# Performance work log

Measured on AMD Instinct MI355X. Metric: run time of the kernel, lower is better.

## Reference

```python
import jax, jax.numpy as jnp
import numpy as np
import math

B, S, H, NH = 2, 2048, 1024, 16
DH = H // NH  # 64
REL_VOCAB = 4096  # 2 * (max_position_embeddings // 4)


def setup_inputs() -> dict:
    key = jax.random.key(0)
    ks = jax.random.split(key, 9)
    s = 0.02
    return {
        "hidden_states": jax.random.normal(ks[0], (B, S, H), jnp.float32),
        "attention_mask": jnp.zeros((B, 1, 1, S), jnp.float32),
        "distance_idx": jax.random.randint(ks[1], (S, S), 0, REL_VOCAB),
        "Wq": jax.random.normal(ks[2], (H, H), jnp.float32) * s,
        "bq": jnp.zeros((H,), jnp.float32),
        "Wk": jax.random.normal(ks[3], (H, H), jnp.float32) * s,
        "bk": jnp.zeros((H,), jnp.float32),
        "Wv": jax.random.normal(ks[4], (H, H), jnp.float32) * s,
        "bv": jnp.zeros((H,), jnp.float32),
        "dist_emb": jax.random.normal(ks[5], (REL_VOCAB, NH), jnp.float32) * s,
    }


def _heads(x):
    # [B,S,H] -> [B,NH,S,DH]
    return x.reshape(B, S, NH, DH).transpose(0, 2, 1, 3)


def reference(hidden_states, attention_mask, distance_idx, Wq, bq, Wk, bk, Wv, bv, dist_emb):
    q = _heads(hidden_states @ Wq.T + bq)
    k = _heads(hidden_states @ Wk.T + bk)
    v = _heads(hidden_states @ Wv.T + bv)
    # scores: [B,NH,S,S]
    scores = jnp.einsum("bhqd,bhkd->bhqk", q, k) / math.sqrt(DH)
    # relative_scalar_bias: embed(distance_idx) [S,S,NH] -> [1,NH,S,S]
    bias = dist_emb[distance_idx].transpose(2, 0, 1)[None]
    scores = scores + bias  # attention_scores_terms == 1 -> /sqrt(1)
    scores = scores + attention_mask
    probs = jax.nn.softmax(scores, axis=-1)
    ctx = jnp.einsum("bhqk,bhkd->bhqd", probs, v)
    return ctx.transpose(0, 2, 1, 3).reshape(B, S, H)
```

## Files before the change

### kernel.cpp

```cpp
#include <hip/hip_runtime.h>
#include <hip/hip_bf16.h>

#define B_   2
#define S_   2048
#define H_   1024
#define NH_  16
#define DH_  64

typedef __attribute__((ext_vector_type(8))) __bf16 bf16x8;
typedef __attribute__((ext_vector_type(8))) unsigned short u16x8;
typedef __attribute__((ext_vector_type(4))) float f32x4;

typedef const __attribute__((address_space(1))) unsigned int gu32_t;
typedef __attribute__((address_space(3))) unsigned int su32_t;

static __device__ inline unsigned short f2bf(float x) {
    union { float f; unsigned u; } v; v.f = x;
    unsigned r = v.u + 0x7fffu + ((v.u >> 16) & 1u);
    return (unsigned short)(r >> 16);
}

static __device__ inline unsigned short f2bf_r(float x) {
    union { float f; unsigned u; } v; v.f = x;
    return (unsigned short)((v.u + 0x8000u) >> 16);
}

static __device__ inline float bf2f(unsigned short u) {
    union { unsigned u; float f; } v; v.u = ((unsigned)u) << 16;
    return v.f;
}

static __device__ inline bf16x8 ldfrag(const unsigned short* p) {
    return __builtin_bit_cast(bf16x8, *(const u16x8*)p);
}

__global__ void conv_all(const float* __restrict__ x,
                         const float* __restrict__ Wq, const float* __restrict__ Wk,
                         const float* __restrict__ Wv, const float* __restrict__ demb,
                         unsigned short* __restrict__ xb, unsigned short* __restrict__ wall,
                         unsigned short* __restrict__ dembT) {
    int bid = blockIdx.x, tid = threadIdx.x;
    if (bid < 4096) {
        int i = bid * 256 + tid;
        float4 v = ((const float4*)x)[i];
        ushort4 o;
        o.x = f2bf(v.x); o.y = f2bf(v.y); o.z = f2bf(v.z); o.w = f2bf(v.w);
        ((ushort4*)xb)[i] = o;
    } else if (bid < 7168) {
        int i = (bid - 4096) * 256 + tid;
        int e = i * 4;
        int which = e >> 20;
        int r4 = (e & ((1 << 20) - 1)) >> 2;
        const float* src = which == 0 ? Wq : which == 1 ? Wk : Wv;
        float4 v = ((const float4*)src)[r4];
        ushort4 o;
        o.x = f2bf(v.x); o.y = f2bf(v.y); o.z = f2bf(v.z); o.w = f2bf(v.w);
        ((ushort4*)wall)[i] = o;
    } else {
        int t = (bid - 7168) * 256 + tid;
        int h = t >> 12, e = t & 4095;
        dembT[t] = f2bf(demb[e * 16 + h]);
    }
}

__global__ __launch_bounds__(256) void gemm_qkv(
    const unsigned short* __restrict__ Xb, const unsigned short* __restrict__ Wall,
    const float* __restrict__ bq, const float* __restrict__ bk, const float* __restrict__ bv,
    unsigned short* __restrict__ Q, unsigned short* __restrict__ K, unsigned short* __restrict__ V)
{
    __shared__ unsigned short As[128 * 32];
    __shared__ unsigned short Bs[128 * 32];
    const int tid = threadIdx.x, lane = tid & 63, wv = tid >> 6;
    const int g = lane >> 4, l16 = lane & 15;
    const int wm = wv >> 1, wn = wv & 1;
    const int bm = blockIdx.y, bn = blockIdx.x;

    const int lrow = lane >> 2, lcol = (lane & 3) * 8;

    f32x4 acc[4][4];
    #pragma unroll
    for (int i = 0; i < 4; ++i)
        #pragma unroll
        for (int j = 0; j < 4; ++j) acc[i][j] = (f32x4){0.f, 0.f, 0.f, 0.f};

    for (int kt = 0; kt < 32; ++kt) {
        #pragma unroll
        for (int i = 0; i < 2; ++i) {
            int chunk = wv * 2 + i;
            int row = chunk * 16 + lrow;
            const unsigned short* ga = &Xb[(size_t)(bm * 128 + row) * 1024 + kt * 32 + lcol];
            const unsigned short* gb = &Wall[(size_t)(bn * 128 + row) * 1024 + kt * 32 + lcol];
            __builtin_amdgcn_global_load_lds((gu32_t*)(const void*)ga, (su32_t*)(void*)&As[chunk * 512], 16, 0, 0);
            __builtin_amdgcn_global_load_lds((gu32_t*)(const void*)gb, (su32_t*)(void*)&Bs[chunk * 512], 16, 0, 0);
        }
        __syncthreads();
        bf16x8 a[4], b[4];
        #pragma unroll
        for (int mi = 0; mi < 4; ++mi) a[mi] = ldfrag(&As[(wm * 64 + mi * 16 + l16) * 32 + g * 8]);
        #pragma unroll
        for (int ni = 0; ni < 4; ++ni) b[ni] = ldfrag(&Bs[(wn * 64 + ni * 16 + l16) * 32 + g * 8]);
        #pragma unroll
        for (int mi = 0; mi < 4; ++mi)
            #pragma unroll
            for (int ni = 0; ni < 4; ++ni)
                acc[mi][ni] = __builtin_amdgcn_mfma_f32_16x16x32_bf16(a[mi], b[ni], acc[mi][ni], 0, 0, 0);
        __syncthreads();
    }

    #pragma unroll
    for (int mi = 0; mi < 4; ++mi) {
        #pragma unroll
        for (int ni = 0; ni < 4; ++ni) {
            int gn = bn * 128 + wn * 64 + ni * 16 + l16;
            int which = gn >> 10, nn = gn & 1023;
            int h = nn >> 6, d = nn & 63;
            float bias = which == 0 ? bq[nn] : which == 1 ? bk[nn] : bv[nn];
            unsigned short* dst = which == 0 ? Q : which == 1 ? K : V;
            #pragma unroll
            for (int r = 0; r < 4; ++r) {
                int gm = bm * 128 + wm * 64 + mi * 16 + g * 4 + r;
                int bb = gm >> 11, s = gm & 2047;
                dst[((size_t)(bb * 16 + h) * 2048 + s) * 64 + d] = f2bf(acc[mi][ni][r] + bias);
            }
        }
    }
}

__global__ void transpose_v(const unsigned short* __restrict__ V, unsigned short* __restrict__ VT) {
    __shared__ unsigned short t[64][65];
    int bh = blockIdx.y, st = blockIdx.x, tid = threadIdx.x;
    size_t ib = (size_t)bh * S_ * DH_ + (size_t)st * 64 * 64;
    #pragma unroll
    for (int rep = 0; rep < 16; ++rep) {
        int e = rep * 256 + tid;
        t[e >> 6][e & 63] = V[ib + e];
    }
    __syncthreads();
    size_t ob = (size_t)bh * DH_ * S_ + st * 64;
    #pragma unroll
    for (int rep = 0; rep < 16; ++rep) {
        int e = rep * 256 + tid;
        int d = e >> 6, sl = e & 63;
        VT[ob + (size_t)d * S_ + sl] = t[sl][d];
    }
}

__global__ __launch_bounds__(256, 4) void attn(
    const unsigned short* __restrict__ Q, const unsigned short* __restrict__ K,
    const unsigned short* __restrict__ VT, const int* __restrict__ didx,
    const unsigned short* __restrict__ dembT, const float* __restrict__ mask,
    float* __restrict__ out)
{
    __shared__ unsigned short demb_h[4096];
    __shared__ unsigned short Ks[64 * 64];
    __shared__ unsigned short Vs[64 * 64];
    __shared__ unsigned short Ps[4][16 * 64];
    const int tid = threadIdx.x, lane = tid & 63, w = tid >> 6;
    const int g = lane >> 4, l16 = lane & 15;
    const int h = blockIdx.x, qt = blockIdx.y, b = blockIdx.z;
    const int bh = b * NH_ + h;
    const int qr = qt * 64 + w * 16;

    #pragma unroll
    for (int j = 0; j < 2; ++j) {
        int i = j * 256 + tid;
        *(uint4*)&demb_h[i * 8] = *(const uint4*)&dembT[h * 4096 + i * 8];
    }

    bf16x8 qf[2];
    {
        size_t qbase = ((size_t)bh * S_ + qr + l16) * DH_;
        qf[0] = ldfrag(&Q[qbase + g * 8]);
        qf[1] = ldfrag(&Q[qbase + 32 + g * 8]);
    }

    f32x4 oa[4];
    float lsum[4];
    #pragma unroll
    for (int i = 0; i < 4; ++i) {
        oa[i] = (f32x4){0.f, 0.f, 0.f, 0.f};
        lsum[i] = 0.f;
    }

    const size_t kbase = (size_t)bh * S_ * DH_;
    const size_t vbase = (size_t)bh * DH_ * S_;

    __syncthreads();

    for (int kt = 0; kt < 32; ++kt) {
        #pragma unroll
        for (int j = 0; j < 2; ++j) {
            int e = j * 2048 + tid * 8;
            int r = e >> 6, c = e & 63;
            int sidx = r * 64 + ((((c >> 3) ^ (r & 7))) << 3);
            *(uint4*)&Ks[sidx] = *(const uint4*)&K[kbase + (size_t)kt * 64 * 64 + e];
            *(uint4*)&Vs[sidx] = *(const uint4*)&VT[vbase + (size_t)r * S_ + kt * 64 + c];
        }

        int ei[4][4];
        float mk[4];
        #pragma unroll
        for (int kj = 0; kj < 4; ++kj) {
            int kg = kt * 64 + kj * 16 + l16;
            mk[kj] = mask[b * S_ + kg];
            #pragma unroll
            for (int r = 0; r < 4; ++r) {
                int qg = qr + g * 4 + r;
                ei[kj][r] = didx[qg * S_ + kg];
            }
        }

        __syncthreads();

        f32x4 sc[4];
        #pragma unroll
        for (int kj = 0; kj < 4; ++kj) {
            int row = kj * 16 + l16, m = row & 7;
            bf16x8 kf0 = ldfrag(&Ks[row * 64 + ((g ^ m) << 3)]);
            bf16x8 kf1 = ldfrag(&Ks[row * 64 + (((g + 4) ^ m) << 3)]);
            f32x4 z = (f32x4){0.f, 0.f, 0.f, 0.f};
            z = __builtin_amdgcn_mfma_f32_16x16x32_bf16(qf[0], kf0, z, 0, 0, 0);
            z = __builtin_amdgcn_mfma_f32_16x16x32_bf16(qf[1], kf1, z, 0, 0, 0);
            sc[kj] = z;
        }

        #pragma unroll
        for (int kj = 0; kj < 4; ++kj) {
            #pragma unroll
            for (int r = 0; r < 4; ++r) {
                float bm = bf2f(demb_h[ei[kj][r]]) + mk[kj];
                float p = __expf(fmaf(sc[kj][r], 0.125f, bm));
                lsum[r] += p;
                int row = g * 4 + r;
                int idx = row * 64 + ((((kj * 2 + (l16 >> 3)) ^ (row & 7))) << 3) + (l16 & 7);
                Ps[w][idx] = f2bf_r(p);
            }
        }

        int pm = l16 & 7;
        bf16x8 pf0 = ldfrag(&Ps[w][l16 * 64 + ((g ^ pm) << 3)]);
        bf16x8 pf1 = ldfrag(&Ps[w][l16 * 64 + (((g + 4) ^ pm) << 3)]);
        #pragma unroll
        for (int dt = 0; dt < 4; ++dt) {
            int row = dt * 16 + l16, m = row & 7;
            bf16x8 vf0 = ldfrag(&Vs[row * 64 + ((g ^ m) << 3)]);
            bf16x8 vf1 = ldfrag(&Vs[row * 64 + (((g + 4) ^ m) << 3)]);
            oa[dt] = __builtin_amdgcn_mfma_f32_16x16x32_bf16(pf0, vf0, oa[dt], 0, 0, 0);
            oa[dt] = __builtin_amdgcn_mfma_f32_16x16x32_bf16(pf1, vf1, oa[dt], 0, 0, 0);
        }
        __syncthreads();
    }

    float linv[4];
    #pragma unroll
    for (int r = 0; r < 4; ++r) {
        float s = lsum[r];
        s += __shfl_xor(s, 1);
        s += __shfl_xor(s, 2);
        s += __shfl_xor(s, 4);
        s += __shfl_xor(s, 8);
        linv[r] = __builtin_amdgcn_rcpf(s);
    }

    #pragma unroll
    for (int dt = 0; dt < 4; ++dt) {
        #pragma unroll
        for (int r = 0; r < 4; ++r) {
            int s = qr + g * 4 + r;
            int d = dt * 16 + l16;
            out[((size_t)b * S_ + s) * H_ + h * DH_ + d] = oa[dt][r] * linv[r];
        }
    }
}

extern "C" void kernel_launch(void* const* d_in, const int* in_sizes, int n_in,
                              void* d_out, int out_size, void* d_ws, size_t ws_size,
                              hipStream_t stream) {
    const float* hidden = (const float*)d_in[0];
    const float* mask   = (const float*)d_in[1];
    const int*   didx   = (const int*)d_in[2];
    const float* Wq     = (const float*)d_in[3];
    const float* bq     = (const float*)d_in[4];
    const float* Wk     = (const float*)d_in[5];
    const float* bk     = (const float*)d_in[6];
    const float* Wv     = (const float*)d_in[7];
    const float* bv     = (const float*)d_in[8];
    const float* demb   = (const float*)d_in[9];
    float* out = (float*)d_out;

    unsigned short* ws = (unsigned short*)d_ws;
    unsigned short* Xb   = ws;
    unsigned short* Wall = Xb + 4096 * 1024;
    unsigned short* Qb   = Wall + 3072 * 1024;
    unsigned short* Kb   = Qb + 4194304;
    unsigned short* Vb   = Kb + 4194304;
    unsigned short* VTb  = Vb + 4194304;
    unsigned short* DembT = VTb + 4194304;

    conv_all<<<7424, 256, 0, stream>>>(hidden, Wq, Wk, Wv, demb, Xb, Wall, DembT);
    gemm_qkv<<<dim3(24, 32), 256, 0, stream>>>(Xb, Wall, bq, bk, bv, Qb, Kb, Vb);
    transpose_v<<<dim3(32, 32), 256, 0, stream>>>(Vb, VTb);
    attn<<<dim3(16, 32, 2), 256, 0, stream>>>(Qb, Kb, VTb, didx, DembT, mask, out);
}
```

Baseline: 221.4 us.

## Register-prefetch next K/V tile and bias indices; raise wave priority around MFMAs

```diff
diff --git a/kernel.cpp b/kernel.cpp
--- a/kernel.cpp
+++ b/kernel.cpp
@@ -185,6 +185,32 @@
     const size_t kbase = (size_t)bh * S_ * DH_;
     const size_t vbase = (size_t)bh * DH_ * S_;
 
+    uint4 kreg[2], vreg[2];
+    int   ei[4][4];
+    float mk[4];
+
+    auto load_kv = [&](int kt) {
+        #pragma unroll
+        for (int j = 0; j < 2; ++j) {
+            int e = j * 2048 + tid * 8;
+            int r = e >> 6, c = e & 63;
+            kreg[j] = *(const uint4*)&K[kbase + (size_t)kt * 64 * 64 + e];
+            vreg[j] = *(const uint4*)&VT[vbase + (size_t)r * S_ + kt * 64 + c];
+        }
+    };
+
+    load_kv(0);
+    #pragma unroll
+    for (int kj = 0; kj < 4; ++kj) {
+        int kg = kj * 16 + l16;
+        mk[kj] = mask[b * S_ + kg];
+        #pragma unroll
+        for (int r = 0; r < 4; ++r) {
+            int qg = qr + g * 4 + r;
+            ei[kj][r] = didx[qg * S_ + kg];
+        }
+    }
+
     __syncthreads();
 
     for (int kt = 0; kt < 32; ++kt) {
@@ -193,26 +219,35 @@
             int e = j * 2048 + tid * 8;
             int r = e >> 6, c = e & 63;
             int sidx = r * 64 + ((((c >> 3) ^ (r & 7))) << 3);
-            *(uint4*)&Ks[sidx] = *(const uint4*)&K[kbase + (size_t)kt * 64 * 64 + e];
-            *(uint4*)&Vs[sidx] = *(const uint4*)&VT[vbase + (size_t)r * S_ + kt * 64 + c];
-        }
-
-        int ei[4][4];
-        float mk[4];
+            *(uint4*)&Ks[sidx] = kreg[j];
+            *(uint4*)&Vs[sidx] = vreg[j];
+        }
+        __syncthreads();
+
+        const int ktn = (kt + 1) & 31;
+        load_kv(ktn);
+        int ein[4][4];
+        float mkn[4];
         #pragma unroll
         for (int kj = 0; kj < 4; ++kj) {
-            int kg = kt * 64 + kj * 16 + l16;
-            mk[kj] = mask[b * S_ + kg];
+            int kg = ktn * 64 + kj * 16 + l16;
+            mkn[kj] = mask[b * S_ + kg];
             #pragma unroll
             for (int r = 0; r < 4; ++r) {
                 int qg = qr + g * 4 + r;
-                ei[kj][r] = didx[qg * S_ + kg];
+                ein[kj][r] = didx[qg * S_ + kg];
             }
         }
 
-        __syncthreads();
+        float bm[4][4];
+        #pragma unroll
+        for (int kj = 0; kj < 4; ++kj)
+            #pragma unroll
+            for (int r = 0; r < 4; ++r)
+                bm[kj][r] = bf2f(demb_h[ei[kj][r]]) + mk[kj];
 
         f32x4 sc[4];
+        __builtin_amdgcn_s_setprio(1);
         #pragma unroll
         for (int kj = 0; kj < 4; ++kj) {
             int row = kj * 16 + l16, m = row & 7;
@@ -223,13 +258,13 @@
             z = __builtin_amdgcn_mfma_f32_16x16x32_bf16(qf[1], kf1, z, 0, 0, 0);
             sc[kj] = z;
         }
+        __builtin_amdgcn_s_setprio(0);
 
         #pragma unroll
         for (int kj = 0; kj < 4; ++kj) {
             #pragma unroll
             for (int r = 0; r < 4; ++r) {
-                float bm = bf2f(demb_h[ei[kj][r]]) + mk[kj];
-                float p = __expf(fmaf(sc[kj][r], 0.125f, bm));
+                float p = __expf(fmaf(sc[kj][r], 0.125f, bm[kj][r]));
                 lsum[r] += p;
                 int row = g * 4 + r;
                 int idx = row * 64 + ((((kj * 2 + (l16 >> 3)) ^ (row & 7))) << 3) + (l16 & 7);
@@ -240,6 +275,7 @@
         int pm = l16 & 7;
         bf16x8 pf0 = ldfrag(&Ps[w][l16 * 64 + ((g ^ pm) << 3)]);
         bf16x8 pf1 = ldfrag(&Ps[w][l16 * 64 + (((g + 4) ^ pm) << 3)]);
+        __builtin_amdgcn_s_setprio(1);
         #pragma unroll
         for (int dt = 0; dt < 4; ++dt) {
             int row = dt * 16 + l16, m = row & 7;
@@ -248,7 +284,15 @@
             oa[dt] = __builtin_amdgcn_mfma_f32_16x16x32_bf16(pf0, vf0, oa[dt], 0, 0, 0);
             oa[dt] = __builtin_amdgcn_mfma_f32_16x16x32_bf16(pf1, vf1, oa[dt], 0, 0, 0);
         }
+        __builtin_amdgcn_s_setprio(0);
         __syncthreads();
+
+        #pragma unroll
+        for (int kj = 0; kj < 4; ++kj) {
+            mk[kj] = mkn[kj];
+            #pragma unroll
+            for (int r = 0; r < 4; ++r) ei[kj][r] = ein[kj][r];
+        }
     }
 
     float linv[4];
```

Measured after the change: 360.5 us. 62.8% more time.

## Split score computation by key columns per wave and share P tile across block

Applied to the files above, without the earlier changes.

```diff
diff --git a/kernel.cpp b/kernel.cpp
--- a/kernel.cpp
+++ b/kernel.cpp
@@ -59,7 +59,7 @@
     } else {
         int t = (bid - 7168) * 256 + tid;
         int h = t >> 12, e = t & 4095;
-        dembT[t] = f2bf(demb[e * 16 + h]);
+        dembT[t] = f2bf(demb[e * 16 + h] * 1.4426950408889634f);
     }
 }
 
@@ -154,7 +154,7 @@
     __shared__ unsigned short demb_h[4096];
     __shared__ unsigned short Ks[64 * 64];
     __shared__ unsigned short Vs[64 * 64];
-    __shared__ unsigned short Ps[4][16 * 64];
+    __shared__ unsigned short Ps[64 * 64];
     const int tid = threadIdx.x, lane = tid & 63, w = tid >> 6;
     const int g = lane >> 4, l16 = lane & 15;
     const int h = blockIdx.x, qt = blockIdx.y, b = blockIdx.z;
@@ -167,20 +167,23 @@
         *(uint4*)&demb_h[i * 8] = *(const uint4*)&dembT[h * 4096 + i * 8];
     }
 
-    bf16x8 qf[2];
-    {
-        size_t qbase = ((size_t)bh * S_ + qr + l16) * DH_;
-        qf[0] = ldfrag(&Q[qbase + g * 8]);
-        qf[1] = ldfrag(&Q[qbase + 32 + g * 8]);
-    }
+    bf16x8 qf[4][2];
+    #pragma unroll
+    for (int qtile = 0; qtile < 4; ++qtile) {
+        size_t qbase = ((size_t)bh * S_ + qt * 64 + qtile * 16 + l16) * DH_;
+        qf[qtile][0] = ldfrag(&Q[qbase + g * 8]);
+        qf[qtile][1] = ldfrag(&Q[qbase + 32 + g * 8]);
+    }
+
+    u16x8 ou;
+    #pragma unroll
+    for (int i = 0; i < 8; ++i) ou[i] = 0x3F80;
+    const bf16x8 onesf = __builtin_bit_cast(bf16x8, ou);
 
     f32x4 oa[4];
-    float lsum[4];
-    #pragma unroll
-    for (int i = 0; i < 4; ++i) {
-        oa[i] = (f32x4){0.f, 0.f, 0.f, 0.f};
-        lsum[i] = 0.f;
-    }
+    f32x4 lacc = (f32x4){0.f, 0.f, 0.f, 0.f};
+    #pragma unroll
+    for (int i = 0; i < 4; ++i) oa[i] = (f32x4){0.f, 0.f, 0.f, 0.f};
 
     const size_t kbase = (size_t)bh * S_ * DH_;
     const size_t vbase = (size_t)bh * DH_ * S_;
@@ -197,49 +200,50 @@
             *(uint4*)&Vs[sidx] = *(const uint4*)&VT[vbase + (size_t)r * S_ + kt * 64 + c];
         }
 
+        const int kg = kt * 64 + w * 16 + l16;
+        float mk = mask[b * S_ + kg];
         int ei[4][4];
-        float mk[4];
-        #pragma unroll
-        for (int kj = 0; kj < 4; ++kj) {
-            int kg = kt * 64 + kj * 16 + l16;
-            mk[kj] = mask[b * S_ + kg];
+        #pragma unroll
+        for (int qtile = 0; qtile < 4; ++qtile) {
             #pragma unroll
             for (int r = 0; r < 4; ++r) {
-                int qg = qr + g * 4 + r;
-                ei[kj][r] = didx[qg * S_ + kg];
+                int qg = qt * 64 + qtile * 16 + g * 4 + r;
+                ei[qtile][r] = didx[qg * S_ + kg];
             }
         }
-
-        __syncthreads();
-
-        f32x4 sc[4];
-        #pragma unroll
-        for (int kj = 0; kj < 4; ++kj) {
-            int row = kj * 16 + l16, m = row & 7;
-            bf16x8 kf0 = ldfrag(&Ks[row * 64 + ((g ^ m) << 3)]);
-            bf16x8 kf1 = ldfrag(&Ks[row * 64 + (((g + 4) ^ m) << 3)]);
+        __syncthreads();
+
+        const int krow = w * 16 + l16, km = krow & 7;
+        bf16x8 kf0 = ldfrag(&Ks[krow * 64 + ((g ^ km) << 3)]);
+        bf16x8 kf1 = ldfrag(&Ks[krow * 64 + (((g + 4) ^ km) << 3)]);
+        const float mkl = mk * 1.4426950408889634f;
+        const int pcol = w * 16 + l16;
+        const int chunkx = pcol >> 3, coff = pcol & 7;
+
+        __builtin_amdgcn_s_setprio(1);
+        #pragma unroll
+        for (int qtile = 0; qtile < 4; ++qtile) {
             f32x4 z = (f32x4){0.f, 0.f, 0.f, 0.f};
-            z = __builtin_amdgcn_mfma_f32_16x16x32_bf16(qf[0], kf0, z, 0, 0, 0);
-            z = __builtin_amdgcn_mfma_f32_16x16x32_bf16(qf[1], kf1, z, 0, 0, 0);
-            sc[kj] = z;
-        }
-
-        #pragma unroll
-        for (int kj = 0; kj < 4; ++kj) {
+            z = __builtin_amdgcn_mfma_f32_16x16x32_bf16(qf[qtile][0], kf0, z, 0, 0, 0);
+            z = __builtin_amdgcn_mfma_f32_16x16x32_bf16(qf[qtile][1], kf1, z, 0, 0, 0);
             #pragma unroll
             for (int r = 0; r < 4; ++r) {
-                float bm = bf2f(demb_h[ei[kj][r]]) + mk[kj];
-                float p = __expf(fmaf(sc[kj][r], 0.125f, bm));
-                lsum[r] += p;
-                int row = g * 4 + r;
-                int idx = row * 64 + ((((kj * 2 + (l16 >> 3)) ^ (row & 7))) << 3) + (l16 & 7);
-                Ps[w][idx] = f2bf_r(p);
+                float bm = bf2f(demb_h[ei[qtile][r]]) + mkl;
+                float p = __builtin_amdgcn_exp2f(fmaf(z[r], 0.18033688011112042f, bm));
+                int q = qtile * 16 + g * 4 + r;
+                int idx = q * 64 + (((chunkx ^ (q & 7))) << 3) + coff;
+                Ps[idx] = f2bf_r(p);
             }
         }
-
-        int pm = l16 & 7;
-        bf16x8 pf0 = ldfrag(&Ps[w][l16 * 64 + ((g ^ pm) << 3)]);
-        bf16x8 pf1 = ldfrag(&Ps[w][l16 * 64 + (((g + 4) ^ pm) << 3)]);
+        __builtin_amdgcn_s_setprio(0);
+        __syncthreads();
+
+        const int prow = w * 16 + l16, pm = prow & 7;
+        bf16x8 pf0 = ldfrag(&Ps[prow * 64 + ((g ^ pm) << 3)]);
+        bf16x8 pf1 = ldfrag(&Ps[prow * 64 + (((g + 4) ^ pm) << 3)]);
+        __builtin_amdgcn_s_setprio(1);
+        lacc = __builtin_amdgcn_mfma_f32_16x16x32_bf16(pf0, onesf, lacc, 0, 0, 0);
+        lacc = __builtin_amdgcn_mfma_f32_16x16x32_bf16(pf1, onesf, lacc, 0, 0, 0);
         #pragma unroll
         for (int dt = 0; dt < 4; ++dt) {
             int row = dt * 16 + l16, m = row & 7;
@@ -248,19 +252,13 @@
             oa[dt] = __builtin_amdgcn_mfma_f32_16x16x32_bf16(pf0, vf0, oa[dt], 0, 0, 0);
             oa[dt] = __builtin_amdgcn_mfma_f32_16x16x32_bf16(pf1, vf1, oa[dt], 0, 0, 0);
         }
+        __builtin_amdgcn_s_setprio(0);
         __syncthreads();
     }
 
     float linv[4];
     #pragma unroll
-    for (int r = 0; r < 4; ++r) {
-        float s = lsum[r];
-        s += __shfl_xor(s, 1);
-        s += __shfl_xor(s, 2);
-        s += __shfl_xor(s, 4);
-        s += __shfl_xor(s, 8);
-        linv[r] = __builtin_amdgcn_rcpf(s);
-    }
+    for (int r = 0; r < 4; ++r) linv[r] = __builtin_amdgcn_rcpf(lacc[r]);
 
     #pragma unroll
     for (int dt = 0; dt < 4; ++dt) {
```

Result: no change. 222.0 us (+0.3%).

## Double-buffer LDS tiles in QKV GEMM to overlap global loads with MFMA

Applied to the files above, without the earlier changes.

```diff
diff --git a/kernel.cpp b/kernel.cpp
--- a/kernel.cpp
+++ b/kernel.cpp
@@ -68,8 +68,8 @@
     const float* __restrict__ bq, const float* __restrict__ bk, const float* __restrict__ bv,
     unsigned short* __restrict__ Q, unsigned short* __restrict__ K, unsigned short* __restrict__ V)
 {
-    __shared__ unsigned short As[128 * 32];
-    __shared__ unsigned short Bs[128 * 32];
+    __shared__ unsigned short As[2][128 * 32];
+    __shared__ unsigned short Bs[2][128 * 32];
     const int tid = threadIdx.x, lane = tid & 63, wv = tid >> 6;
     const int g = lane >> 4, l16 = lane & 15;
     const int wm = wv >> 1, wn = wv & 1;
@@ -83,29 +83,46 @@
         #pragma unroll
         for (int j = 0; j < 4; ++j) acc[i][j] = (f32x4){0.f, 0.f, 0.f, 0.f};
 
+    const int chunk0 = wv * 2, chunk1 = wv * 2 + 1;
+    const size_t arow0 = (size_t)(bm * 128 + chunk0 * 16 + lrow) * 1024 + lcol;
+    const size_t arow1 = (size_t)(bm * 128 + chunk1 * 16 + lrow) * 1024 + lcol;
+    const size_t brow0 = (size_t)(bn * 128 + chunk0 * 16 + lrow) * 1024 + lcol;
+    const size_t brow1 = (size_t)(bn * 128 + chunk1 * 16 + lrow) * 1024 + lcol;
+
+#define STAGE(BUF, KT)                                                                      \
+    {                                                                                       \
+        __builtin_amdgcn_global_load_lds((gu32_t*)(const void*)&Xb[arow0 + (KT) * 32],      \
+            (su32_t*)(void*)&As[BUF][chunk0 * 512], 16, 0, 0);                              \
+        __builtin_amdgcn_global_load_lds((gu32_t*)(const void*)&Wall[brow0 + (KT) * 32],    \
+            (su32_t*)(void*)&Bs[BUF][chunk0 * 512], 16, 0, 0);                              \
+        __builtin_amdgcn_global_load_lds((gu32_t*)(const void*)&Xb[arow1 + (KT) * 32],      \
+            (su32_t*)(void*)&As[BUF][chunk1 * 512], 16, 0, 0);                              \
+        __builtin_amdgcn_global_load_lds((gu32_t*)(const void*)&Wall[brow1 + (KT) * 32],    \
+            (su32_t*)(void*)&Bs[BUF][chunk1 * 512], 16, 0, 0);                              \
+    }
+
+    STAGE(0, 0)
+    __syncthreads();
+
+    int cur = 0;
     for (int kt = 0; kt < 32; ++kt) {
-        #pragma unroll
-        for (int i = 0; i < 2; ++i) {
-            int chunk = wv * 2 + i;
-            int row = chunk * 16 + lrow;
-            const unsigned short* ga = &Xb[(size_t)(bm * 128 + row) * 1024 + kt * 32 + lcol];
-            const unsigned short* gb = &Wall[(size_t)(bn * 128 + row) * 1024 + kt * 32 + lcol];
-            __builtin_amdgcn_global_load_lds((gu32_t*)(const void*)ga, (su32_t*)(void*)&As[chunk * 512], 16, 0, 0);
-            __builtin_amdgcn_global_load_lds((gu32_t*)(const void*)gb, (su32_t*)(void*)&Bs[chunk * 512], 16, 0, 0);
-        }
-        __syncthreads();
+        if (kt < 31) STAGE(cur ^ 1, kt + 1)
+
         bf16x8 a[4], b[4];
         #pragma unroll
-        for (int mi = 0; mi < 4; ++mi) a[mi] = ldfrag(&As[(wm * 64 + mi * 16 + l16) * 32 + g * 8]);
-        #pragma unroll
-        for (int ni = 0; ni < 4; ++ni) b[ni] = ldfrag(&Bs[(wn * 64 + ni * 16 + l16) * 32 + g * 8]);
+        for (int mi = 0; mi < 4; ++mi) a[mi] = ldfrag(&As[cur][(wm * 64 + mi * 16 + l16) * 32 + g * 8]);
+        #pragma unroll
+        for (int ni = 0; ni < 4; ++ni) b[ni] = ldfrag(&Bs[cur][(wn * 64 + ni * 16 + l16) * 32 + g * 8]);
         #pragma unroll
         for (int mi = 0; mi < 4; ++mi)
             #pragma unroll
             for (int ni = 0; ni < 4; ++ni)
                 acc[mi][ni] = __builtin_amdgcn_mfma_f32_16x16x32_bf16(a[mi], b[ni], acc[mi][ni], 0, 0, 0);
+
         __syncthreads();
-    }
+        cur ^= 1;
+    }
+#undef STAGE
 
     #pragma unroll
     for (int mi = 0; mi < 4; ++mi) {
```

New measurement: 226.4 us. +2.3%, slower.
